# Kernel optimization log

Measured on AMD Instinct MI355X. Metric: run time of the kernel, lower is better.

The kernel has to match this reference:

```python
import jax, jax.numpy as jnp
import numpy as np

T, H, I, E, TOPK = 1024, 1024, 2048, 8, 2


def setup_inputs() -> dict:
    key = jax.random.key(0)
    k1, k2, k3, k4, k5, k6 = jax.random.split(key, 6)
    hidden_states = jax.random.normal(k1, (T, H), dtype=jnp.float32)
    expert_affinities = jax.random.uniform(k2, (T, E), dtype=jnp.float32)
    expert_index = jax.random.randint(k3, (T, TOPK), 0, E, dtype=jnp.int64)
    # Expert GLU MLP weights: gate/up [E,H,I], down [E,I,H]
    w_gate = jax.random.normal(k4, (E, H, I), dtype=jnp.float32) / np.sqrt(H)
    w_up = jax.random.normal(k5, (E, H, I), dtype=jnp.float32) / np.sqrt(H)
    w_down = jax.random.normal(k6, (E, I, H), dtype=jnp.float32) / np.sqrt(I)
    return {
        "hidden_states": hidden_states,
        "expert_affinities": expert_affinities,
        "expert_index": expert_index,
        "w_gate": w_gate,
        "w_up": w_up,
        "w_down": w_down,
        "seq_len": T,
    }


def reference(hidden_states, expert_affinities, expert_index, w_gate, w_up, w_down, seq_len):
    # Gather top-k affinities and renormalize (normalize_top_k_affinities=True)
    topk_aff = jnp.take_along_axis(expert_affinities, expert_index, axis=1)  # [T,K]
    topk_aff = topk_aff / jnp.sum(topk_aff, axis=1, keepdims=True)
    # Dense combine weights [T,E] (scatter of normalized top-k affinities)
    t_idx = jnp.arange(hidden_states.shape[0])[:, None]
    combine = jnp.zeros((hidden_states.shape[0], w_gate.shape[0]),
                        dtype=hidden_states.dtype).at[t_idx, expert_index].add(topk_aff)
    # GLU expert MLP for all experts (E small, grouped-GEMM form)
    g = jnp.einsum("th,ehi->tei", hidden_states, w_gate)  # [T,E,I]
    u = jnp.einsum("th,ehi->tei", hidden_states, w_up)    # [T,E,I]
    act = jax.nn.silu(g) * u                               # [T,E,I]
    # Down-projection fused with affinity-weighted combine
    out = jnp.einsum("tei,eih,te->th", act, w_down, combine)  # [T,H]
    return out
```

## Files before the change

kernel.cpp:

```cpp
#include <hip/hip_runtime.h>
#include <hip/hip_bf16.h>
#include <math.h>

#define T_ 1024
#define H_ 1024
#define I_ 2048
#define E_ 8
#define NSLOT 2048

#define BM 128
#define BK 32
#define BN1 64
#define BN2 64
#define NCHUNK_CAP 24
#define SPLITK2 2

typedef __attribute__((ext_vector_type(8))) short bf16x8;
typedef __attribute__((ext_vector_type(4))) float f32x4;
typedef __attribute__((ext_vector_type(4))) unsigned uint4v;
typedef __attribute__((ext_vector_type(2))) unsigned uint2v;

#define MFMA_BF16 __builtin_amdgcn_mfma_f32_16x16x32_bf16

__device__ __forceinline__ short f2bf(float f) {
  union { float f; unsigned u; } v; v.f = f;
  unsigned r = v.u + 0x7FFFu + ((v.u >> 16) & 1u);
  return (short)(r >> 16);
}
__device__ __forceinline__ unsigned cvtpk(float lo, float hi) {
  unsigned r;
  asm("v_cvt_pk_bf16_f32 %0, %1, %2" : "=v"(r) : "v"(lo), "v"(hi));
  return r;
}
__device__ __forceinline__ void gll16(const void* g, void* l) {
  __builtin_amdgcn_global_load_lds(
      (const __attribute__((address_space(1))) void*)g,
      (__attribute__((address_space(3))) void*)l, 16, 0, 0);
}

__device__ __forceinline__ void pipe_barrier6() {
  __builtin_amdgcn_sched_barrier(0);
  asm volatile("s_waitcnt vmcnt(6) lgkmcnt(0)" ::: "memory");
  __builtin_amdgcn_s_barrier();
  __builtin_amdgcn_sched_barrier(0);
}
__device__ __forceinline__ void pipe_barrier4() {
  __builtin_amdgcn_sched_barrier(0);
  asm volatile("s_waitcnt vmcnt(4) lgkmcnt(0)" ::: "memory");
  __builtin_amdgcn_s_barrier();
  __builtin_amdgcn_sched_barrier(0);
}
__device__ __forceinline__ void drain_barrier() {
  __builtin_amdgcn_sched_barrier(0);
  asm volatile("s_waitcnt vmcnt(0) lgkmcnt(0)" ::: "memory");
  __builtin_amdgcn_s_barrier();
  __builtin_amdgcn_sched_barrier(0);
}

__device__ __forceinline__ int rswz(int row) { return (row >> 1) & 3; }
__device__ __forceinline__ unsigned tile_addr(int row, int g) {
  return (unsigned)(row * 64 + (((g ^ rswz(row)) & 3) << 4));
}

__global__ __launch_bounds__(256) void k_prep(const float* __restrict__ hs,
                                              short* __restrict__ hs_bf) {
  int i = (blockIdx.x * 256 + threadIdx.x) * 8;
  float4 v0 = *(const float4*)&hs[i];
  float4 v1 = *(const float4*)&hs[i + 4];
  uint4v p;
  p.x = cvtpk(v0.x, v0.y); p.y = cvtpk(v0.z, v0.w);
  p.z = cvtpk(v1.x, v1.y); p.w = cvtpk(v1.z, v1.w);
  *(uint4v*)&hs_bf[i] = p;
}

__global__ __launch_bounds__(1024) void k_build(
    const float* __restrict__ aff, const int* __restrict__ eidx,
    int* __restrict__ meta, int* __restrict__ slot_tok, float* __restrict__ slot_w) {
  __shared__ int cnt[E_];
  __shared__ int soff[E_ + 1];
  int t = threadIdx.x;
  if (t < E_) cnt[t] = 0;
  __syncthreads();
  int e0 = eidx[t * 2 + 0];
  int e1 = eidx[t * 2 + 1];
  float a0 = aff[t * E_ + e0];
  float a1 = aff[t * E_ + e1];
  float inv = 1.0f / (a0 + a1);
  int r0 = atomicAdd(&cnt[e0], 1);
  int r1 = atomicAdd(&cnt[e1], 1);
  __syncthreads();
  if (t == 0) {
    int s = 0;
    for (int e = 0; e < E_; ++e) { soff[e] = s; s += cnt[e]; }
    soff[E_] = s;
    int nc = 0;
    for (int e = 0; e < E_; ++e)
      for (int c = soff[e]; c < soff[e] + cnt[e]; c += BM)
        meta[16 + nc++] = e | (c << 8);
    meta[9] = nc;
  }
  __syncthreads();
  if (t <= E_) meta[t] = soff[t];
  int s0 = soff[e0] + r0;
  int s1 = soff[e1] + r1;
  slot_tok[s0] = t; slot_w[s0] = a0 * inv;
  slot_tok[s1] = t; slot_w[s1] = a1 * inv;
}

__global__ __launch_bounds__(256, 2) void k_gemm1(
    const short* __restrict__ hs_bf, const float* __restrict__ wg,
    const float* __restrict__ wu, const int* __restrict__ meta,
    const int* __restrict__ slot_tok, short* __restrict__ act) {
  int nch = meta[9];
  if (blockIdx.y >= nch) return;
  int ck = meta[16 + blockIdx.y];
  int e = ck & 255;
  int row0 = ck >> 8;
  int rows = min(BM, meta[1 + e] - row0);
  int i0 = blockIdx.x * BN1;

  __shared__ short sA[4][BM * BK];
  __shared__ short sB[2][2][BN1 * BK];

  int tid = threadIdx.x;
  int lane = tid & 63;
  int w = tid >> 6;
  int wm = w >> 1, wn = w & 1;
  int lr = lane & 15;
  int g = lane >> 4;

  const float* wgE = wg + (size_t)e * H_ * I_;
  const float* wuE = wu + (size_t)e * H_ * I_;

  int r_a0 = 32 * w + (lane >> 2);
  int r_a1 = r_a0 + 16;
  int tok0 = slot_tok[row0 + min(r_a0, rows - 1)];
  int tok1 = slot_tok[row0 + min(r_a1, rows - 1)];
  const short* srcA0 = hs_bf + (size_t)tok0 * H_ + ((((lane & 3) ^ rswz(r_a0)) & 3) << 3);
  const short* srcA1 = hs_bf + (size_t)tok1 * H_ + ((((lane & 3) ^ rswz(r_a1)) & 3) << 3);

  int mat = tid >> 7;
  int kq = (tid >> 4) & 7;
  int nq = tid & 15;
  const float* srcB = (mat ? wuE : wgE) + (size_t)(4 * kq) * I_ + i0 + 4 * nq;

  f32x4 accg[4][2], accu[4][2];
#pragma unroll
  for (int mf = 0; mf < 4; ++mf)
#pragma unroll
    for (int nf = 0; nf < 2; ++nf) {
      accg[mf][nf] = (f32x4){0.f, 0.f, 0.f, 0.f};
      accu[mf][nf] = (f32x4){0.f, 0.f, 0.f, 0.f};
    }

  f32x4 bs0[4], bs1[4];

  const int NT = H_ / BK;

  gll16(srcA0, &sA[0][(32 * w) * 32]);
  gll16(srcA1, &sA[0][(32 * w + 16) * 32]);
#pragma unroll
  for (int j = 0; j < 4; ++j) bs0[j] = *(const f32x4*)(srcB + (size_t)j * I_);
  gll16(srcA0 + BK, &sA[1][(32 * w) * 32]);
  gll16(srcA1 + BK, &sA[1][(32 * w + 16) * 32]);
#pragma unroll
  for (int j = 0; j < 4; ++j) bs1[j] = *(const f32x4*)(srcB + (size_t)(BK + j) * I_);
  {
    char* dst = (char*)&sB[0][mat][0];
#pragma unroll
    for (int c = 0; c < 4; ++c) {
      int n = 4 * nq + c;
      uint2v wv;
      wv.x = cvtpk(bs0[0][c], bs0[1][c]);
      wv.y = cvtpk(bs0[2][c], bs0[3][c]);
      *(uint2v*)(dst + tile_addr(n, kq >> 1) + ((kq & 1) << 3)) = wv;
    }
  }
  drain_barrier();

#define G1_ITER(U, bsL, bsC) do {                                              \
    int t_ = base + (U);                                                       \
    const char* curA = (const char*)&sA[t_ & 3][0];                            \
    if (t_ + 2 < NT) {                                                         \
      short* nxtA = &sA[(t_ + 2) & 3][0];                                      \
      gll16(srcA0 + (size_t)(t_ + 2) * BK, nxtA + (32 * w) * 32);              \
      gll16(srcA1 + (size_t)(t_ + 2) * BK, nxtA + (32 * w + 16) * 32);         \
      const float* sb = srcB + (size_t)(t_ + 2) * BK * I_;                     \
      bsL[0] = *(const f32x4*)(sb);                                            \
      bsL[1] = *(const f32x4*)(sb + I_);                                       \
      bsL[2] = *(const f32x4*)(sb + 2 * I_);                                   \
      bsL[3] = *(const f32x4*)(sb + 3 * I_);                                   \
    }                                                                          \
    bf16x8 a0 = *(const bf16x8*)(curA + tile_addr(wm * 64 + lr, g));           \
    bf16x8 a1 = *(const bf16x8*)(curA + tile_addr(wm * 64 + 16 + lr, g));      \
    bf16x8 a2 = *(const bf16x8*)(curA + tile_addr(wm * 64 + 32 + lr, g));      \
    bf16x8 a3 = *(const bf16x8*)(curA + tile_addr(wm * 64 + 48 + lr, g));      \
    const char* pg = (const char*)&sB[(U)][0][0];                              \
    const char* pu = (const char*)&sB[(U)][1][0];                              \
    unsigned ob0 = tile_addr(wn * 32 + lr, g);                                 \
    unsigned ob1 = tile_addr(wn * 32 + 16 + lr, g);                            \
    bf16x8 g0 = *(const bf16x8*)(pg + ob0);                                    \
    bf16x8 g1 = *(const bf16x8*)(pg + ob1);                                    \
    bf16x8 u0 = *(const bf16x8*)(pu + ob0);                                    \
    bf16x8 u1 = *(const bf16x8*)(pu + ob1);                                    \
    accg[0][0] = MFMA_BF16(a0, g0, accg[0][0], 0, 0, 0);                       \
    accg[0][1] = MFMA_BF16(a0, g1, accg[0][1], 0, 0, 0);                       \
    accg[1][0] = MFMA_BF16(a1, g0, accg[1][0], 0, 0, 0);                       \
    accg[1][1] = MFMA_BF16(a1, g1, accg[1][1], 0, 0, 0);                       \
    accg[2][0] = MFMA_BF16(a2, g0, accg[2][0], 0, 0, 0);                       \
    accg[2][1] = MFMA_BF16(a2, g1, accg[2][1], 0, 0, 0);                       \
    accg[3][0] = MFMA_BF16(a3, g0, accg[3][0], 0, 0, 0);                       \
    accg[3][1] = MFMA_BF16(a3, g1, accg[3][1], 0, 0, 0);                       \
    accu[0][0] = MFMA_BF16(a0, u0, accu[0][0], 0, 0, 0);                       \
    accu[0][1] = MFMA_BF16(a0, u1, accu[0][1], 0, 0, 0);                       \
    accu[1][0] = MFMA_BF16(a1, u0, accu[1][0], 0, 0, 0);                       \
    accu[1][1] = MFMA_BF16(a1, u1, accu[1][1], 0, 0, 0);                       \
    accu[2][0] = MFMA_BF16(a2, u0, accu[2][0], 0, 0, 0);                       \
    accu[2][1] = MFMA_BF16(a2, u1, accu[2][1], 0, 0, 0);                       \
    accu[3][0] = MFMA_BF16(a3, u0, accu[3][0], 0, 0, 0);                       \
    accu[3][1] = MFMA_BF16(a3, u1, accu[3][1], 0, 0, 0);                       \
    if (t_ + 1 < NT) {                                                         \
      char* dst = (char*)&sB[(U) ^ 1][mat][0];                                 \
      _Pragma("unroll")                                                        \
      for (int c = 0; c < 4; ++c) {                                            \
        int n = 4 * nq + c;                                                    \
        uint2v wv;                                                             \
        wv.x = cvtpk(bsC[0][c], bsC[1][c]);                                    \
        wv.y = cvtpk(bsC[2][c], bsC[3][c]);                                    \
        *(uint2v*)(dst + tile_addr(n, kq >> 1) + ((kq & 1) << 3)) = wv;        \
      }                                                                        \
    }                                                                          \
    pipe_barrier6();                                                           \
  } while (0)

  for (int base = 0; base < NT; base += 2) {
    G1_ITER(0, bs0, bs1);
    G1_ITER(1, bs1, bs0);
  }
#undef G1_ITER

#pragma unroll
  for (int mf = 0; mf < 4; ++mf) {
#pragma unroll
    for (int r = 0; r < 4; ++r) {
      int m = wm * 64 + mf * 16 + g * 4 + r;
      if (m < rows) {
#pragma unroll
        for (int nf = 0; nf < 2; ++nf) {
          float gv = accg[mf][nf][r];
          float uv = accu[mf][nf][r];
          float sg = 1.0f / (1.0f + __expf(-gv));
          act[(size_t)(row0 + m) * I_ + i0 + wn * 32 + nf * 16 + lr] = f2bf(gv * sg * uv);
        }
      }
    }
  }
}

__global__ __launch_bounds__(256, 2) void k_gemm2(
    const short* __restrict__ act, const float* __restrict__ wd,
    const int* __restrict__ meta, const int* __restrict__ slot_tok,
    const float* __restrict__ slot_w, float* __restrict__ out) {
  int nch = meta[9];
  if (blockIdx.y >= nch) return;
  int ck = meta[16 + blockIdx.y];
  int e = ck & 255;
  int row0 = ck >> 8;
  int rows = min(BM, meta[1 + e] - row0);
  int h0 = blockIdx.x * BN2;
  int kbase = blockIdx.z * (I_ / SPLITK2);

  __shared__ short sA[4][BM * BK];
  __shared__ short sB[2][BN2 * BK];

  int tid = threadIdx.x;
  int lane = tid & 63;
  int w = tid >> 6;
  int wm = w >> 1, wn = w & 1;
  int lr = lane & 15;
  int g = lane >> 4;

  const float* wdE = wd + (size_t)e * I_ * H_;

  int isB = (w < 2);
  int kq = (tid >> 4) & 7;
  int nq = tid & 15;
  const float* srcB = wdE + (size_t)(kbase + 4 * kq) * H_ + h0 + 4 * nq;
  int wp = w & 1;
  int r_a = 64 * wp + (lane >> 2);
  const short* srcA[4];
#pragma unroll
  for (int p = 0; p < 4; ++p) {
    int rr = r_a + 16 * p;
    int gs = ((lane & 3) ^ rswz(rr)) & 3;
    srcA[p] = act + (size_t)(row0 + min(rr, rows - 1)) * I_ + kbase + (gs << 3);
  }

  f32x4 acc[4][2];
#pragma unroll
  for (int mf = 0; mf < 4; ++mf)
#pragma unroll
    for (int nf = 0; nf < 2; ++nf)
      acc[mf][nf] = (f32x4){0.f, 0.f, 0.f, 0.f};

  f32x4 bs0[4], bs1[4];

  const int NT = (I_ / SPLITK2) / BK;

  if (isB) {
#pragma unroll
    for (int j = 0; j < 4; ++j) bs0[j] = *(const f32x4*)(srcB + (size_t)j * H_);
#pragma unroll
    for (int j = 0; j < 4; ++j) bs1[j] = *(const f32x4*)(srcB + (size_t)(BK + j) * H_);
  } else {
#pragma unroll
    for (int p = 0; p < 4; ++p)
      gll16(srcA[p], &sA[0][(64 * wp + 16 * p) * 32]);
#pragma unroll
    for (int p = 0; p < 4; ++p)
      gll16(srcA[p] + BK, &sA[1][(64 * wp + 16 * p) * 32]);
  }
  if (isB) {
    char* dst = (char*)&sB[0][0];
#pragma unroll
    for (int c = 0; c < 4; ++c) {
      int n = 4 * nq + c;
      uint2v wv;
      wv.x = cvtpk(bs0[0][c], bs0[1][c]);
      wv.y = cvtpk(bs0[2][c], bs0[3][c]);
      *(uint2v*)(dst + tile_addr(n, kq >> 1) + ((kq & 1) << 3)) = wv;
    }
  }
  drain_barrier();

#define G2_ITER(U, bsL, bsC) do {                                              \
    int t_ = base + (U);                                                       \
    const char* curA = (const char*)&sA[t_ & 3][0];                            \
    if (t_ + 2 < NT) {                                                         \
      if (isB) {                                                               \
        const float* sb = srcB + (size_t)(t_ + 2) * BK * H_;                   \
        bsL[0] = *(const f32x4*)(sb);                                          \
        bsL[1] = *(const f32x4*)(sb + H_);                                     \
        bsL[2] = *(const f32x4*)(sb + 2 * H_);                                 \
        bsL[3] = *(const f32x4*)(sb + 3 * H_);                                 \
      } else {                                                                 \
        short* nxtA = &sA[(t_ + 2) & 3][0];                                    \
        gll16(srcA[0] + (size_t)(t_ + 2) * BK, nxtA + (64 * wp) * 32);         \
        gll16(srcA[1] + (size_t)(t_ + 2) * BK, nxtA + (64 * wp + 16) * 32);    \
        gll16(srcA[2] + (size_t)(t_ + 2) * BK, nxtA + (64 * wp + 32) * 32);    \
        gll16(srcA[3] + (size_t)(t_ + 2) * BK, nxtA + (64 * wp + 48) * 32);    \
      }                                                                        \
    }                                                                          \
    bf16x8 a0 = *(const bf16x8*)(curA + tile_addr(wm * 64 + lr, g));           \
    bf16x8 a1 = *(const bf16x8*)(curA + tile_addr(wm * 64 + 16 + lr, g));      \
    bf16x8 a2 = *(const bf16x8*)(curA + tile_addr(wm * 64 + 32 + lr, g));      \
    bf16x8 a3 = *(const bf16x8*)(curA + tile_addr(wm * 64 + 48 + lr, g));      \
    const char* pb = (const char*)&sB[(U)][0];                                 \
    bf16x8 b0 = *(const bf16x8*)(pb + tile_addr(wn * 32 + lr, g));             \
    bf16x8 b1 = *(const bf16x8*)(pb + tile_addr(wn * 32 + 16 + lr, g));        \
    acc[0][0] = MFMA_BF16(a0, b0, acc[0][0], 0, 0, 0);                         \
    acc[0][1] = MFMA_BF16(a0, b1, acc[0][1], 0, 0, 0);                         \
    acc[1][0] = MFMA_BF16(a1, b0, acc[1][0], 0, 0, 0);                         \
    acc[1][1] = MFMA_BF16(a1, b1, acc[1][1], 0, 0, 0);                         \
    acc[2][0] = MFMA_BF16(a2, b0, acc[2][0], 0, 0, 0);                         \
    acc[2][1] = MFMA_BF16(a2, b1, acc[2][1], 0, 0, 0);                         \
    acc[3][0] = MFMA_BF16(a3, b0, acc[3][0], 0, 0, 0);                         \
    acc[3][1] = MFMA_BF16(a3, b1, acc[3][1], 0, 0, 0);                         \
    if (isB && t_ + 1 < NT) {                                                  \
      char* dst = (char*)&sB[(U) ^ 1][0];                                      \
      _Pragma("unroll")                                                        \
      for (int c = 0; c < 4; ++c) {                                            \
        int n = 4 * nq + c;                                                    \
        uint2v wv;                                                             \
        wv.x = cvtpk(bsC[0][c], bsC[1][c]);                                    \
        wv.y = cvtpk(bsC[2][c], bsC[3][c]);                                    \
        *(uint2v*)(dst + tile_addr(n, kq >> 1) + ((kq & 1) << 3)) = wv;        \
      }                                                                        \
    }                                                                          \
    pipe_barrier4();                                                           \
  } while (0)

  for (int base = 0; base < NT; base += 2) {
    G2_ITER(0, bs0, bs1);
    G2_ITER(1, bs1, bs0);
  }
#undef G2_ITER

#pragma unroll
  for (int mf = 0; mf < 4; ++mf) {
#pragma unroll
    for (int r = 0; r < 4; ++r) {
      int m = wm * 64 + mf * 16 + g * 4 + r;
      if (m < rows) {
        int gs = row0 + m;
        float wc = slot_w[gs];
        int tok = slot_tok[gs];
#pragma unroll
        for (int nf = 0; nf < 2; ++nf)
          atomicAdd(&out[(size_t)tok * H_ + h0 + wn * 32 + nf * 16 + lr],
                    acc[mf][nf][r] * wc);
      }
    }
  }
}

extern "C" void kernel_launch(void* const* d_in, const int* in_sizes, int n_in,
                              void* d_out, int out_size, void* d_ws, size_t ws_size,
                              hipStream_t stream) {
  const float* hs   = (const float*)d_in[0];
  const float* aff  = (const float*)d_in[1];
  const int*   eidx = (const int*)d_in[2];
  const float* wg   = (const float*)d_in[3];
  const float* wu   = (const float*)d_in[4];
  const float* wd   = (const float*)d_in[5];
  float* out = (float*)d_out;

  char* ws = (char*)d_ws;
  int*   meta     = (int*)ws;
  int*   slot_tok = (int*)(ws + 256);
  float* slot_w   = (float*)(ws + 256 + NSLOT * 4);
  short* hs_bf    = (short*)(ws + 256 + NSLOT * 8);
  short* act      = (short*)(ws + 256 + NSLOT * 8 + (size_t)T_ * H_ * 2);

  hipMemsetAsync(d_out, 0, (size_t)out_size * sizeof(float), stream);
  k_build<<<1, T_, 0, stream>>>(aff, eidx, meta, slot_tok, slot_w);
  k_prep<<<(T_ * H_) / (256 * 8), 256, 0, stream>>>(hs, hs_bf);
  k_gemm1<<<dim3(I_ / BN1, NCHUNK_CAP), 256, 0, stream>>>(hs_bf, wg, wu, meta, slot_tok, act);
  k_gemm2<<<dim3(H_ / BN2, NCHUNK_CAP, SPLITK2), 256, 0, stream>>>(act, wd, meta, slot_tok, slot_w, out);
}
```

Measured before the change: 103.1 us.

## Enlarge M tile to 256 rows and reassign warps along M in both expert GEMMs

Raises the row tile from 128 to 256 and narrows the GEMM1 N tile to 32. Each of the four warps now owns a 64-row strip and the full N width, so expert weights are re-read from global memory for fewer row chunks. GEMM2 now has every warp load both A and B and widens the per-warp accumulator to 4x4 MFMA fragments; B loads become float2 and the vmcnt waits are raised to match. The trade-off is fewer blocks along M, which can leave the GPU underoccupied, plus higher register pressure and more LDS.

```diff
diff --git a/kernel.cpp b/kernel.cpp
--- a/kernel.cpp
+++ b/kernel.cpp
@@ -8,11 +8,11 @@
 #define E_ 8
 #define NSLOT 2048
 
-#define BM 128
+#define BM 256
 #define BK 32
-#define BN1 64
+#define BN1 32
 #define BN2 64
-#define NCHUNK_CAP 24
+#define NCHUNK_CAP 16
 #define SPLITK2 2
 
 typedef __attribute__((ext_vector_type(8))) short bf16x8;
@@ -38,15 +38,15 @@
       (__attribute__((address_space(3))) void*)l, 16, 0, 0);
 }
 
-__device__ __forceinline__ void pipe_barrier6() {
-  __builtin_amdgcn_sched_barrier(0);
-  asm volatile("s_waitcnt vmcnt(6) lgkmcnt(0)" ::: "memory");
+__device__ __forceinline__ void pipe_barrier12() {
+  __builtin_amdgcn_sched_barrier(0);
+  asm volatile("s_waitcnt vmcnt(12) lgkmcnt(0)" ::: "memory");
   __builtin_amdgcn_s_barrier();
   __builtin_amdgcn_sched_barrier(0);
 }
-__device__ __forceinline__ void pipe_barrier4() {
-  __builtin_amdgcn_sched_barrier(0);
-  asm volatile("s_waitcnt vmcnt(4) lgkmcnt(0)" ::: "memory");
+__device__ __forceinline__ void pipe_barrier8() {
+  __builtin_amdgcn_sched_barrier(0);
+  asm volatile("s_waitcnt vmcnt(8) lgkmcnt(0)" ::: "memory");
   __builtin_amdgcn_s_barrier();
   __builtin_amdgcn_sched_barrier(0);
 }
@@ -125,24 +125,26 @@
   int tid = threadIdx.x;
   int lane = tid & 63;
   int w = tid >> 6;
-  int wm = w >> 1, wn = w & 1;
   int lr = lane & 15;
   int g = lane >> 4;
 
   const float* wgE = wg + (size_t)e * H_ * I_;
   const float* wuE = wu + (size_t)e * H_ * I_;
 
-  int r_a0 = 32 * w + (lane >> 2);
-  int r_a1 = r_a0 + 16;
-  int tok0 = slot_tok[row0 + min(r_a0, rows - 1)];
-  int tok1 = slot_tok[row0 + min(r_a1, rows - 1)];
-  const short* srcA0 = hs_bf + (size_t)tok0 * H_ + ((((lane & 3) ^ rswz(r_a0)) & 3) << 3);
-  const short* srcA1 = hs_bf + (size_t)tok1 * H_ + ((((lane & 3) ^ rswz(r_a1)) & 3) << 3);
+  int rbase = 64 * w + (lane >> 2);
+  const short* srcA[4];
+#pragma unroll
+  for (int p = 0; p < 4; ++p) {
+    int rr = rbase + 16 * p;
+    int tok = slot_tok[row0 + min(rr, rows - 1)];
+    int gsw = ((lane & 3) ^ rswz(rr)) & 3;
+    srcA[p] = hs_bf + (size_t)tok * H_ + (gsw << 3);
+  }
 
   int mat = tid >> 7;
   int kq = (tid >> 4) & 7;
-  int nq = tid & 15;
-  const float* srcB = (mat ? wuE : wgE) + (size_t)(4 * kq) * I_ + i0 + 4 * nq;
+  int n2 = (tid & 15) * 2;
+  const float* srcB = (mat ? wuE : wgE) + (size_t)(4 * kq) * I_ + i0 + n2;
 
   f32x4 accg[4][2], accu[4][2];
 #pragma unroll
@@ -153,28 +155,25 @@
       accu[mf][nf] = (f32x4){0.f, 0.f, 0.f, 0.f};
     }
 
-  f32x4 bs0[4], bs1[4];
+  float2 bs0[4], bs1[4];
 
   const int NT = H_ / BK;
 
-  gll16(srcA0, &sA[0][(32 * w) * 32]);
-  gll16(srcA1, &sA[0][(32 * w + 16) * 32]);
-#pragma unroll
-  for (int j = 0; j < 4; ++j) bs0[j] = *(const f32x4*)(srcB + (size_t)j * I_);
-  gll16(srcA0 + BK, &sA[1][(32 * w) * 32]);
-  gll16(srcA1 + BK, &sA[1][(32 * w + 16) * 32]);
-#pragma unroll
-  for (int j = 0; j < 4; ++j) bs1[j] = *(const f32x4*)(srcB + (size_t)(BK + j) * I_);
+#pragma unroll
+  for (int p = 0; p < 4; ++p) gll16(srcA[p], &sA[0][(64 * w + 16 * p) * 32]);
+#pragma unroll
+  for (int j = 0; j < 4; ++j) bs0[j] = *(const float2*)(srcB + (size_t)j * I_);
+#pragma unroll
+  for (int p = 0; p < 4; ++p) gll16(srcA[p] + BK, &sA[1][(64 * w + 16 * p) * 32]);
+#pragma unroll
+  for (int j = 0; j < 4; ++j) bs1[j] = *(const float2*)(srcB + (size_t)(BK + j) * I_);
   {
     char* dst = (char*)&sB[0][mat][0];
-#pragma unroll
-    for (int c = 0; c < 4; ++c) {
-      int n = 4 * nq + c;
-      uint2v wv;
-      wv.x = cvtpk(bs0[0][c], bs0[1][c]);
-      wv.y = cvtpk(bs0[2][c], bs0[3][c]);
-      *(uint2v*)(dst + tile_addr(n, kq >> 1) + ((kq & 1) << 3)) = wv;
-    }
+    uint2v wv0, wv1;
+    wv0.x = cvtpk(bs0[0].x, bs0[1].x); wv0.y = cvtpk(bs0[2].x, bs0[3].x);
+    wv1.x = cvtpk(bs0[0].y, bs0[1].y); wv1.y = cvtpk(bs0[2].y, bs0[3].y);
+    *(uint2v*)(dst + tile_addr(n2, kq >> 1) + ((kq & 1) << 3)) = wv0;
+    *(uint2v*)(dst + tile_addr(n2 + 1, kq >> 1) + ((kq & 1) << 3)) = wv1;
   }
   drain_barrier();
 
@@ -183,22 +182,24 @@
     const char* curA = (const char*)&sA[t_ & 3][0];                            \
     if (t_ + 2 < NT) {                                                         \
       short* nxtA = &sA[(t_ + 2) & 3][0];                                      \
-      gll16(srcA0 + (size_t)(t_ + 2) * BK, nxtA + (32 * w) * 32);              \
-      gll16(srcA1 + (size_t)(t_ + 2) * BK, nxtA + (32 * w + 16) * 32);         \
+      gll16(srcA[0] + (size_t)(t_ + 2) * BK, nxtA + (64 * w) * 32);            \
+      gll16(srcA[1] + (size_t)(t_ + 2) * BK, nxtA + (64 * w + 16) * 32);       \
+      gll16(srcA[2] + (size_t)(t_ + 2) * BK, nxtA + (64 * w + 32) * 32);       \
+      gll16(srcA[3] + (size_t)(t_ + 2) * BK, nxtA + (64 * w + 48) * 32);       \
       const float* sb = srcB + (size_t)(t_ + 2) * BK * I_;                     \
-      bsL[0] = *(const f32x4*)(sb);                                            \
-      bsL[1] = *(const f32x4*)(sb + I_);                                       \
-      bsL[2] = *(const f32x4*)(sb + 2 * I_);                                   \
-      bsL[3] = *(const f32x4*)(sb + 3 * I_);                                   \
+      bsL[0] = *(const float2*)(sb);                                           \
+      bsL[1] = *(const float2*)(sb + I_);                                      \
+      bsL[2] = *(const float2*)(sb + 2 * I_);                                  \
+      bsL[3] = *(const float2*)(sb + 3 * I_);                                  \
     }                                                                          \
-    bf16x8 a0 = *(const bf16x8*)(curA + tile_addr(wm * 64 + lr, g));           \
-    bf16x8 a1 = *(const bf16x8*)(curA + tile_addr(wm * 64 + 16 + lr, g));      \
-    bf16x8 a2 = *(const bf16x8*)(curA + tile_addr(wm * 64 + 32 + lr, g));      \
-    bf16x8 a3 = *(const bf16x8*)(curA + tile_addr(wm * 64 + 48 + lr, g));      \
+    bf16x8 a0 = *(const bf16x8*)(curA + tile_addr(64 * w + lr, g));            \
+    bf16x8 a1 = *(const bf16x8*)(curA + tile_addr(64 * w + 16 + lr, g));       \
+    bf16x8 a2 = *(const bf16x8*)(curA + tile_addr(64 * w + 32 + lr, g));       \
+    bf16x8 a3 = *(const bf16x8*)(curA + tile_addr(64 * w + 48 + lr, g));       \
     const char* pg = (const char*)&sB[(U)][0][0];                              \
     const char* pu = (const char*)&sB[(U)][1][0];                              \
-    unsigned ob0 = tile_addr(wn * 32 + lr, g);                                 \
-    unsigned ob1 = tile_addr(wn * 32 + 16 + lr, g);                            \
+    unsigned ob0 = tile_addr(lr, g);                                           \
+    unsigned ob1 = tile_addr(16 + lr, g);                                      \
     bf16x8 g0 = *(const bf16x8*)(pg + ob0);                                    \
     bf16x8 g1 = *(const bf16x8*)(pg + ob1);                                    \
     bf16x8 u0 = *(const bf16x8*)(pu + ob0);                                    \
@@ -221,16 +222,13 @@
     accu[3][1] = MFMA_BF16(a3, u1, accu[3][1], 0, 0, 0);                       \
     if (t_ + 1 < NT) {                                                         \
       char* dst = (char*)&sB[(U) ^ 1][mat][0];                                 \
-      _Pragma("unroll")                                                        \
-      for (int c = 0; c < 4; ++c) {                                            \
-        int n = 4 * nq + c;                                                    \
-        uint2v wv;                                                             \
-        wv.x = cvtpk(bsC[0][c], bsC[1][c]);                                    \
-        wv.y = cvtpk(bsC[2][c], bsC[3][c]);                                    \
-        *(uint2v*)(dst + tile_addr(n, kq >> 1) + ((kq & 1) << 3)) = wv;        \
-      }                                                                        \
+      uint2v wv0, wv1;                                                         \
+      wv0.x = cvtpk(bsC[0].x, bsC[1].x); wv0.y = cvtpk(bsC[2].x, bsC[3].x);    \
+      wv1.x = cvtpk(bsC[0].y, bsC[1].y); wv1.y = cvtpk(bsC[2].y, bsC[3].y);    \
+      *(uint2v*)(dst + tile_addr(n2, kq >> 1) + ((kq & 1) << 3)) = wv0;        \
+      *(uint2v*)(dst + tile_addr(n2 + 1, kq >> 1) + ((kq & 1) << 3)) = wv1;    \
     }                                                                          \
-    pipe_barrier6();                                                           \
+    pipe_barrier12();                                                          \
   } while (0)
 
   for (int base = 0; base < NT; base += 2) {
@@ -243,14 +241,14 @@
   for (int mf = 0; mf < 4; ++mf) {
 #pragma unroll
     for (int r = 0; r < 4; ++r) {
-      int m = wm * 64 + mf * 16 + g * 4 + r;
+      int m = 64 * w + mf * 16 + g * 4 + r;
       if (m < rows) {
 #pragma unroll
         for (int nf = 0; nf < 2; ++nf) {
           float gv = accg[mf][nf][r];
           float uv = accu[mf][nf][r];
           float sg = 1.0f / (1.0f + __expf(-gv));
-          act[(size_t)(row0 + m) * I_ + i0 + wn * 32 + nf * 16 + lr] = f2bf(gv * sg * uv);
+          act[(size_t)(row0 + m) * I_ + i0 + nf * 16 + lr] = f2bf(gv * sg * uv);
         }
       }
     }
@@ -276,60 +274,49 @@
   int tid = threadIdx.x;
   int lane = tid & 63;
   int w = tid >> 6;
-  int wm = w >> 1, wn = w & 1;
   int lr = lane & 15;
   int g = lane >> 4;
 
   const float* wdE = wd + (size_t)e * I_ * H_;
 
-  int isB = (w < 2);
-  int kq = (tid >> 4) & 7;
-  int nq = tid & 15;
-  const float* srcB = wdE + (size_t)(kbase + 4 * kq) * H_ + h0 + 4 * nq;
-  int wp = w & 1;
-  int r_a = 64 * wp + (lane >> 2);
+  int rbase = 64 * w + (lane >> 2);
   const short* srcA[4];
 #pragma unroll
   for (int p = 0; p < 4; ++p) {
-    int rr = r_a + 16 * p;
-    int gs = ((lane & 3) ^ rswz(rr)) & 3;
-    srcA[p] = act + (size_t)(row0 + min(rr, rows - 1)) * I_ + kbase + (gs << 3);
-  }
-
-  f32x4 acc[4][2];
+    int rr = rbase + 16 * p;
+    int gsw = ((lane & 3) ^ rswz(rr)) & 3;
+    srcA[p] = act + (size_t)(row0 + min(rr, rows - 1)) * I_ + kbase + (gsw << 3);
+  }
+  int kq = tid >> 5;
+  int n2 = (tid & 31) * 2;
+  const float* srcB = wdE + (size_t)(kbase + 4 * kq) * H_ + h0 + n2;
+
+  f32x4 acc[4][4];
 #pragma unroll
   for (int mf = 0; mf < 4; ++mf)
 #pragma unroll
-    for (int nf = 0; nf < 2; ++nf)
+    for (int nf = 0; nf < 4; ++nf)
       acc[mf][nf] = (f32x4){0.f, 0.f, 0.f, 0.f};
 
-  f32x4 bs0[4], bs1[4];
+  float2 bs0[4], bs1[4];
 
   const int NT = (I_ / SPLITK2) / BK;
 
-  if (isB) {
-#pragma unroll
-    for (int j = 0; j < 4; ++j) bs0[j] = *(const f32x4*)(srcB + (size_t)j * H_);
-#pragma unroll
-    for (int j = 0; j < 4; ++j) bs1[j] = *(const f32x4*)(srcB + (size_t)(BK + j) * H_);
-  } else {
-#pragma unroll
-    for (int p = 0; p < 4; ++p)
-      gll16(srcA[p], &sA[0][(64 * wp + 16 * p) * 32]);
-#pragma unroll
-    for (int p = 0; p < 4; ++p)
-      gll16(srcA[p] + BK, &sA[1][(64 * wp + 16 * p) * 32]);
-  }
-  if (isB) {
+#pragma unroll
+  for (int p = 0; p < 4; ++p) gll16(srcA[p], &sA[0][(64 * w + 16 * p) * 32]);
+#pragma unroll
+  for (int j = 0; j < 4; ++j) bs0[j] = *(const float2*)(srcB + (size_t)j * H_);
+#pragma unroll
+  for (int p = 0; p < 4; ++p) gll16(srcA[p] + BK, &sA[1][(64 * w + 16 * p) * 32]);
+#pragma unroll
+  for (int j = 0; j < 4; ++j) bs1[j] = *(const float2*)(srcB + (size_t)(BK + j) * H_);
+  {
     char* dst = (char*)&sB[0][0];
-#pragma unroll
-    for (int c = 0; c < 4; ++c) {
-      int n = 4 * nq + c;
-      uint2v wv;
-      wv.x = cvtpk(bs0[0][c], bs0[1][c]);
-      wv.y = cvtpk(bs0[2][c], bs0[3][c]);
-      *(uint2v*)(dst + tile_addr(n, kq >> 1) + ((kq & 1) << 3)) = wv;
-    }
+    uint2v wv0, wv1;
+    wv0.x = cvtpk(bs0[0].x, bs0[1].x); wv0.y = cvtpk(bs0[2].x, bs0[3].x);
+    wv1.x = cvtpk(bs0[0].y, bs0[1].y); wv1.y = cvtpk(bs0[2].y, bs0[3].y);
+    *(uint2v*)(dst + tile_addr(n2, kq >> 1) + ((kq & 1) << 3)) = wv0;
+    *(uint2v*)(dst + tile_addr(n2 + 1, kq >> 1) + ((kq & 1) << 3)) = wv1;
   }
   drain_barrier();
 
@@ -337,47 +324,51 @@
     int t_ = base + (U);                                                       \
     const char* curA = (const char*)&sA[t_ & 3][0];                            \
     if (t_ + 2 < NT) {                                                         \
-      if (isB) {                                                               \
-        const float* sb = srcB + (size_t)(t_ + 2) * BK * H_;                   \
-        bsL[0] = *(const f32x4*)(sb);                                          \
-        bsL[1] = *(const f32x4*)(sb + H_);                                     \
-        bsL[2] = *(const f32x4*)(sb + 2 * H_);                                 \
-        bsL[3] = *(const f32x4*)(sb + 3 * H_);                                 \
-      } else {                                                                 \
-        short* nxtA = &sA[(t_ + 2) & 3][0];                                    \
-        gll16(srcA[0] + (size_t)(t_ + 2) * BK, nxtA + (64 * wp) * 32);         \
-        gll16(srcA[1] + (size_t)(t_ + 2) * BK, nxtA + (64 * wp + 16) * 32);    \
-        gll16(srcA[2] + (size_t)(t_ + 2) * BK, nxtA + (64 * wp + 32) * 32);    \
-        gll16(srcA[3] + (size_t)(t_ + 2) * BK, nxtA + (64 * wp + 48) * 32);    \
-      }                                                                        \
+      short* nxtA = &sA[(t_ + 2) & 3][0];                                      \
+      gll16(srcA[0] + (size_t)(t_ + 2) * BK, nxtA + (64 * w) * 32);            \
+      gll16(srcA[1] + (size_t)(t_ + 2) * BK, nxtA + (64 * w + 16) * 32);       \
+      gll16(srcA[2] + (size_t)(t_ + 2) * BK, nxtA + (64 * w + 32) * 32);       \
+      gll16(srcA[3] + (size_t)(t_ + 2) * BK, nxtA + (64 * w + 48) * 32);       \
+      const float* sb = srcB + (size_t)(t_ + 2) * BK * H_;                     \
+      bsL[0] = *(const float2*)(sb);                                           \
+      bsL[1] = *(const float2*)(sb + H_);                                      \
+      bsL[2] = *(const float2*)(sb + 2 * H_);                                  \
+      bsL[3] = *(const float2*)(sb + 3 * H_);                                  \
     }                                                                          \
-    bf16x8 a0 = *(const bf16x8*)(curA + tile_addr(wm * 64 + lr, g));           \
-    bf16x8 a1 = *(const bf16x8*)(curA + tile_addr(wm * 64 + 16 + lr, g));      \
-    bf16x8 a2 = *(const bf16x8*)(curA + tile_addr(wm * 64 + 32 + lr, g));      \
-    bf16x8 a3 = *(const bf16x8*)(curA + tile_addr(wm * 64 + 48 + lr, g));      \
+    bf16x8 a0 = *(const bf16x8*)(curA + tile_addr(64 * w + lr, g));            \
+    bf16x8 a1 = *(const bf16x8*)(curA + tile_addr(64 * w + 16 + lr, g));       \
+    bf16x8 a2 = *(const bf16x8*)(curA + tile_addr(64 * w + 32 + lr, g));       \
+    bf16x8 a3 = *(const bf16x8*)(curA + tile_addr(64 * w + 48 + lr, g));       \
     const char* pb = (const char*)&sB[(U)][0];                                 \
-    bf16x8 b0 = *(const bf16x8*)(pb + tile_addr(wn * 32 + lr, g));             \
-    bf16x8 b1 = *(const bf16x8*)(pb + tile_addr(wn * 32 + 16 + lr, g));        \
+    bf16x8 b0 = *(const bf16x8*)(pb + tile_addr(lr, g));                       \
+    bf16x8 b1 = *(const bf16x8*)(pb + tile_addr(16 + lr, g));                  \
+    bf16x8 b2 = *(const bf16x8*)(pb + tile_addr(32 + lr, g));                  \
+    bf16x8 b3 = *(const bf16x8*)(pb + tile_addr(48 + lr, g));                  \
     acc[0][0] = MFMA_BF16(a0, b0, acc[0][0], 0, 0, 0);                         \
     acc[0][1] = MFMA_BF16(a0, b1, acc[0][1], 0, 0, 0);                         \
+    acc[0][2] = MFMA_BF16(a0, b2, acc[0][2], 0, 0, 0);                         \
+    acc[0][3] = MFMA_BF16(a0, b3, acc[0][3], 0, 0, 0);                         \
     acc[1][0] = MFMA_BF16(a1, b0, acc[1][0], 0, 0, 0);                         \
     acc[1][1] = MFMA_BF16(a1, b1, acc[1][1], 0, 0, 0);                         \
+    acc[1][2] = MFMA_BF16(a1, b2, acc[1][2], 0, 0, 0);                         \
+    acc[1][3] = MFMA_BF16(a1, b3, acc[1][3], 0, 0, 0);                         \
     acc[2][0] = MFMA_BF16(a2, b0, acc[2][0], 0, 0, 0);                         \
     acc[2][1] = MFMA_BF16(a2, b1, acc[2][1], 0, 0, 0);                         \
+    acc[2][2] = MFMA_BF16(a2, b2, acc[2][2], 0, 0, 0);                         \
+    acc[2][3] = MFMA_BF16(a2, b3, acc[2][3], 0, 0, 0);                         \
     acc[3][0] = MFMA_BF16(a3, b0, acc[3][0], 0, 0, 0);                         \
     acc[3][1] = MFMA_BF16(a3, b1, acc[3][1], 0, 0, 0);                         \
-    if (isB && t_ + 1 < NT) {                                                  \
+    acc[3][2] = MFMA_BF16(a3, b2, acc[3][2], 0, 0, 0);                         \
+    acc[3][3] = MFMA_BF16(a3, b3, acc[3][3], 0, 0, 0);                         \
+    if (t_ + 1 < NT) {                                                         \
       char* dst = (char*)&sB[(U) ^ 1][0];                                      \
-      _Pragma("unroll")                                                        \
-      for (int c = 0; c < 4; ++c) {                                            \
-        int n = 4 * nq + c;                                                    \
-        uint2v wv;                                                             \
-        wv.x = cvtpk(bsC[0][c], bsC[1][c]);                                    \
-        wv.y = cvtpk(bsC[2][c], bsC[3][c]);                                    \
-        *(uint2v*)(dst + tile_addr(n, kq >> 1) + ((kq & 1) << 3)) = wv;        \
-      }                                                                        \
+      uint2v wv0, wv1;                                                         \
+      wv0.x = cvtpk(bsC[0].x, bsC[1].x); wv0.y = cvtpk(bsC[2].x, bsC[3].x);    \
+      wv1.x = cvtpk(bsC[0].y, bsC[1].y); wv1.y = cvtpk(bsC[2].y, bsC[3].y);    \
+      *(uint2v*)(dst + tile_addr(n2, kq >> 1) + ((kq & 1) << 3)) = wv0;        \
+      *(uint2v*)(dst + tile_addr(n2 + 1, kq >> 1) + ((kq & 1) << 3)) = wv1;    \
     }                                                                          \
-    pipe_barrier4();                                                           \
+    pipe_barrier8();                                                           \
   } while (0)
 
   for (int base = 0; base < NT; base += 2) {
@@ -390,14 +381,14 @@
   for (int mf = 0; mf < 4; ++mf) {
 #pragma unroll
     for (int r = 0; r < 4; ++r) {
-      int m = wm * 64 + mf * 16 + g * 4 + r;
+      int m = 64 * w + mf * 16 + g * 4 + r;
       if (m < rows) {
         int gs = row0 + m;
         float wc = slot_w[gs];
         int tok = slot_tok[gs];
 #pragma unroll
-        for (int nf = 0; nf < 2; ++nf)
-          atomicAdd(&out[(size_t)tok * H_ + h0 + wn * 32 + nf * 16 + lr],
+        for (int nf = 0; nf < 4; ++nf)
+          atomicAdd(&out[(size_t)tok * H_ + h0 + nf * 16 + lr],
                     acc[mf][nf][r] * wc);
       }
     }
```

After: 123.0 us. 19.3% more time.
